# Kernel optimization log

Measured on AMD Instinct MI355X. Metric: run time of the kernel, lower is better.

The kernel has to match this reference:

```python
import jax, jax.numpy as jnp
import numpy as np

EPS = 1e-8  # torch F.cosine_similarity eps


def setup_inputs() -> dict:
    key = jax.random.key(0)
    k1, k2, k3 = jax.random.split(key, 3)
    bn, cn, dim = 4096, 8192, 1024
    x = jax.random.normal(k1, (bn, dim), dtype=jnp.float32)
    positive = jax.random.normal(k2, (bn, dim), dtype=jnp.float32)
    negative = jax.random.normal(k3, (cn, dim), dtype=jnp.float32)
    return {"x": x, "positive": positive, "negative": negative}


def reference(x, positive, negative):
    bn = x.shape[0]
    nx = jnp.linalg.norm(x, axis=1)          # (bn,)
    npos = jnp.linalg.norm(positive, axis=1)  # (bn,)
    nneg = jnp.linalg.norm(negative, axis=1)  # (cn,)
    # positive cosine similarity, torch-style eps clamp on norm product
    sim = jnp.sum(x * positive, axis=1) / jnp.maximum(nx * npos, EPS)  # (bn,)
    # negative cosine similarities via one matmul instead of (bn,cn,dim) repeats
    neg_sim = (x @ negative.T) / jnp.maximum(nx[:, None] * nneg[None, :], EPS)  # (bn,cn)
    p = jnp.exp(sim) / jnp.sum(jnp.exp(neg_sim), axis=1)  # (bn,)
    loss = -jnp.sum(jnp.log(p)) / bn
    return loss
```

## Files before the change

kernel.cpp:

```cpp
#include <hip/hip_runtime.h>
#include <stdint.h>
#include <stddef.h>

#define DIM 1024
#define EPS 1e-8f

typedef __attribute__((ext_vector_type(4))) float f32x4;
typedef __attribute__((ext_vector_type(2))) long longx2;

__device__ __forceinline__ void async_copy16(const void* g, void* l) {
    __builtin_amdgcn_global_load_lds(
        (__attribute__((address_space(1))) void*)const_cast<void*>(g),
        (__attribute__((address_space(3))) void*)(l), 16, 0, 0);
}

#define PIPE_SYNC(N) asm volatile("s_waitcnt vmcnt(" #N ")\n\ts_barrier" ::: "memory")

__global__ __launch_bounds__(256)
void prep_all(const float* __restrict__ x, const float* __restrict__ pos,
              const float* __restrict__ neg,
              unsigned char* __restrict__ Xn, unsigned char* __restrict__ Nn,
              float* __restrict__ simOut, float* __restrict__ rowsum, int bn) {
    const int lane = threadIdx.x & 63;
    const int wave = threadIdx.x >> 6;
    const int grow = blockIdx.x * 4 + wave;
    const bool isX = grow < bn;
    const int row  = isX ? grow : grow - bn;
    const float* src = isX ? x : neg;
    unsigned char* dst = isX ? Xn : Nn;

    const float4* s = (const float4*)(src + (size_t)row * DIM);
    float4 xv[4], pv[4];
    float sxx = 0.f, spp = 0.f, sxp = 0.f;
#pragma unroll
    for (int i = 0; i < 4; i++) {
        xv[i] = s[lane + 64 * i];
        sxx += xv[i].x * xv[i].x + xv[i].y * xv[i].y + xv[i].z * xv[i].z + xv[i].w * xv[i].w;
    }
    if (isX) {
        const float4* p = (const float4*)(pos + (size_t)row * DIM);
#pragma unroll
        for (int i = 0; i < 4; i++) {
            pv[i] = p[lane + 64 * i];
            spp += pv[i].x * pv[i].x + pv[i].y * pv[i].y + pv[i].z * pv[i].z + pv[i].w * pv[i].w;
            sxp += xv[i].x * pv[i].x + xv[i].y * pv[i].y + xv[i].z * pv[i].z + xv[i].w * pv[i].w;
        }
#pragma unroll
        for (int off = 1; off < 64; off <<= 1) {
            sxx += __shfl_xor(sxx, off);
            spp += __shfl_xor(spp, off);
            sxp += __shfl_xor(sxp, off);
        }
    } else {
#pragma unroll
        for (int off = 1; off < 64; off <<= 1) sxx += __shfl_xor(sxx, off);
    }
    const float nx  = sqrtf(sxx);
    const float inv = (nx > 0.f) ? (16.f / nx) : 0.f;
    if (isX && lane == 0) {
        const float np = sqrtf(spp);
        simOut[row] = sxp / fmaxf(nx * np, EPS);
        rowsum[row] = 0.f;
    }
    unsigned int t;
    t = __builtin_amdgcn_cvt_pk_fp8_f32(xv[0].x * inv, xv[0].y * inv, 0, false);
    unsigned int q0 = __builtin_amdgcn_cvt_pk_fp8_f32(xv[0].z * inv, xv[0].w * inv, t, true);
    t = __builtin_amdgcn_cvt_pk_fp8_f32(xv[1].x * inv, xv[1].y * inv, 0, false);
    unsigned int q1 = __builtin_amdgcn_cvt_pk_fp8_f32(xv[1].z * inv, xv[1].w * inv, t, true);
    t = __builtin_amdgcn_cvt_pk_fp8_f32(xv[2].x * inv, xv[2].y * inv, 0, false);
    unsigned int q2 = __builtin_amdgcn_cvt_pk_fp8_f32(xv[2].z * inv, xv[2].w * inv, t, true);
    t = __builtin_amdgcn_cvt_pk_fp8_f32(xv[3].x * inv, xv[3].y * inv, 0, false);
    unsigned int q3 = __builtin_amdgcn_cvt_pk_fp8_f32(xv[3].z * inv, xv[3].w * inv, t, true);

    const int m  = lane & 3;
    const int d0 = (m & 1) * 32 + (m >> 1) * 8;
    unsigned char* wbase = dst + (size_t)row * DIM + (lane >> 2) * 64;
    *(unsigned long long*)(wbase + d0)      = ((unsigned long long)q1 << 32) | q0;
    *(unsigned long long*)(wbase + d0 + 16) = ((unsigned long long)q3 << 32) | q2;
}

__global__ __launch_bounds__(256)
void gemm_exp_rowsum(const unsigned char* __restrict__ Xn,
                     const unsigned char* __restrict__ Nn,
                     float* __restrict__ rowsum) {
    constexpr int KB   = DIM;
    constexpr int BK   = 64;
    constexpr int BUFB = 128 * BK;
    __shared__ __align__(16) unsigned char Ash[3][BUFB];
    __shared__ __align__(16) unsigned char Bsh[3][BUFB];

    const int tid  = threadIdx.x;
    const int lane = tid & 63;
    const int wave = tid >> 6;
    const int rowBase = blockIdx.y * 128;
    const int colBase = blockIdx.x * 128;

    const int srow   = lane >> 2;
    const int schunk = (lane & 3) ^ ((srow >> 1) & 3);
    const unsigned char* gA = Xn + (size_t)(rowBase + wave * 16 + srow) * KB + schunk * 16;
    const unsigned char* gB = Nn + (size_t)(colBase + wave * 16 + srow) * KB + schunk * 16;
    const int lgrp0 = (wave * 16) * BK;
    const int lgrp1 = (wave * 16 + 64) * BK;

    const f32x4 fz = {0.f, 0.f, 0.f, 0.f};
    f32x4 acc[4][4];
#pragma unroll
    for (int mi = 0; mi < 4; mi++)
#pragma unroll
        for (int ni = 0; ni < 4; ni++) acc[mi][ni] = fz;

    const int m0   = (wave >> 1) * 64;
    const int n0   = (wave & 1) * 64;
    const int quad = lane >> 4;
    const int mrow = lane & 15;
    const int kx   = (mrow >> 1) & 3;

    int aoff[4], boff[4];
#pragma unroll
    for (int i = 0; i < 4; i++) {
        aoff[i] = (m0 + i * 16 + mrow) * BK + ((quad ^ kx) << 4);
        boff[i] = (n0 + i * 16 + mrow) * BK + ((quad ^ kx) << 4);
    }

#define STAGE(buf, stg)                                                  \
    do {                                                                 \
        const int kq = (stg) * BK;                                       \
        async_copy16(gA + kq,            &Ash[buf][lgrp0]);              \
        async_copy16(gA + 64 * KB + kq,  &Ash[buf][lgrp1]);              \
        async_copy16(gB + kq,            &Bsh[buf][lgrp0]);              \
        async_copy16(gB + 64 * KB + kq,  &Bsh[buf][lgrp1]);              \
    } while (0)

#define COMPUTE(buf)                                                     \
    do {                                                                 \
        longx2 a2[4], b2[4];                                             \
        _Pragma("unroll")                                                \
        for (int i = 0; i < 4; i++) {                                    \
            a2[i] = *(const longx2*)&Ash[buf][aoff[i]];                  \
            b2[i] = *(const longx2*)&Bsh[buf][boff[i]];                  \
        }                                                                \
        _Pragma("unroll")                                                \
        for (int mi = 0; mi < 4; mi++)                                   \
            _Pragma("unroll")                                            \
            for (int ni = 0; ni < 4; ni++) {                             \
                acc[mi][ni] = __builtin_amdgcn_mfma_f32_16x16x32_fp8_fp8( \
                    a2[mi].x, b2[ni].x, acc[mi][ni], 0, 0, 0);           \
                acc[mi][ni] = __builtin_amdgcn_mfma_f32_16x16x32_fp8_fp8( \
                    a2[mi].y, b2[ni].y, acc[mi][ni], 0, 0, 0);           \
            }                                                            \
    } while (0)

    STAGE(0, 0);
    STAGE(1, 1);
    for (int it = 0; it < 4; it++) {
        const int s = 3 * it + 2;
        PIPE_SYNC(4); STAGE(2, s);     COMPUTE(0);
        PIPE_SYNC(4); STAGE(0, s + 1); COMPUTE(1);
        PIPE_SYNC(4); STAGE(1, s + 2); COMPUTE(2);
    }
    PIPE_SYNC(4); STAGE(2, 14); COMPUTE(0);
    PIPE_SYNC(4); STAGE(0, 15); COMPUTE(1);
    PIPE_SYNC(4);               COMPUTE(2);
    PIPE_SYNC(0);               COMPUTE(0);
#undef STAGE
#undef COMPUTE

#pragma unroll
    for (int mi = 0; mi < 4; mi++) {
        float rs0 = 0.f, rs1 = 0.f, rs2 = 0.f, rs3 = 0.f;
#pragma unroll
        for (int ni = 0; ni < 4; ni++) {
            rs0 += __expf(acc[mi][ni].x * 0.00390625f);
            rs1 += __expf(acc[mi][ni].y * 0.00390625f);
            rs2 += __expf(acc[mi][ni].z * 0.00390625f);
            rs3 += __expf(acc[mi][ni].w * 0.00390625f);
        }
#pragma unroll
        for (int off = 1; off < 16; off <<= 1) {
            rs0 += __shfl_xor(rs0, off);
            rs1 += __shfl_xor(rs1, off);
            rs2 += __shfl_xor(rs2, off);
            rs3 += __shfl_xor(rs3, off);
        }
        if ((lane & 15) == 0) {
            const int r = rowBase + m0 + mi * 16 + quad * 4;
            atomicAdd(&rowsum[r + 0], rs0);
            atomicAdd(&rowsum[r + 1], rs1);
            atomicAdd(&rowsum[r + 2], rs2);
            atomicAdd(&rowsum[r + 3], rs3);
        }
    }
}

__global__ __launch_bounds__(1024)
void loss_kernel(const float* __restrict__ rowsum, const float* __restrict__ sim,
                 float* __restrict__ out, int bn) {
    const int tid  = threadIdx.x;
    const int lane = tid & 63;
    const int wave = tid >> 6;
    float acc = 0.f;
    for (int i = tid; i < bn; i += 1024) acc += logf(rowsum[i]) - sim[i];
#pragma unroll
    for (int off = 1; off < 64; off <<= 1) acc += __shfl_xor(acc, off);
    __shared__ float red[16];
    if (lane == 0) red[wave] = acc;
    __syncthreads();
    if (tid == 0) {
        float t = 0.f;
#pragma unroll
        for (int i = 0; i < 16; i++) t += red[i];
        out[0] = t / (float)bn;
    }
}

extern "C" void kernel_launch(void* const* d_in, const int* in_sizes, int n_in,
                              void* d_out, int out_size, void* d_ws, size_t ws_size,
                              hipStream_t stream) {
    const float* x   = (const float*)d_in[0];
    const float* pos = (const float*)d_in[1];
    const float* neg = (const float*)d_in[2];
    const int bn = in_sizes[0] / DIM;
    const int cn = in_sizes[2] / DIM;

    unsigned char* Xn = (unsigned char*)d_ws;
    unsigned char* Nn = Xn + (size_t)bn * DIM;
    float* sim    = (float*)(Nn + (size_t)cn * DIM);
    float* rowsum = sim + bn;

    prep_all<<<dim3((bn + cn) / 4), dim3(256), 0, stream>>>(x, pos, neg, Xn, Nn, sim, rowsum, bn);
    gemm_exp_rowsum<<<dim3(cn / 128, bn / 128), dim3(256), 0, stream>>>(Xn, Nn, rowsum);
    loss_kernel<<<dim3(1), dim3(1024), 0, stream>>>(rowsum, sim, (float*)d_out, bn);
}
```

Before: 166.8 us.

## Double-buffer GEMM pipeline and fuse final loss reduction into last block

The GEMM main loop goes from three LDS buffers to two. It waits on lgkmcnt after the fragment reads so the next async stage can be issued into the just-read buffer before the MFMAs. The separate single-block loss kernel is removed: a global done counter (reset in prep) elects the last finishing GEMM block to do the log-sum reduction. This saves a kernel launch and halves LDS use per block, which may raise occupancy, but it shortens prefetch distance and adds a serial tail reduction on one 256-thread block.

```diff
diff --git a/kernel.cpp b/kernel.cpp
--- a/kernel.cpp
+++ b/kernel.cpp
@@ -15,12 +15,14 @@
 }
 
 #define PIPE_SYNC(N) asm volatile("s_waitcnt vmcnt(" #N ")\n\ts_barrier" ::: "memory")
+#define LGK0() asm volatile("s_waitcnt lgkmcnt(0)" ::: "memory")
 
 __global__ __launch_bounds__(256)
 void prep_all(const float* __restrict__ x, const float* __restrict__ pos,
               const float* __restrict__ neg,
               unsigned char* __restrict__ Xn, unsigned char* __restrict__ Nn,
-              float* __restrict__ simOut, float* __restrict__ rowsum, int bn) {
+              float* __restrict__ simOut, float* __restrict__ rowsum,
+              int* __restrict__ done, int bn) {
     const int lane = threadIdx.x & 63;
     const int wave = threadIdx.x >> 6;
     const int grow = blockIdx.x * 4 + wave;
@@ -61,6 +63,7 @@
         const float np = sqrtf(spp);
         simOut[row] = sxp / fmaxf(nx * np, EPS);
         rowsum[row] = 0.f;
+        if (row == 0) *done = 0;
     }
     unsigned int t;
     t = __builtin_amdgcn_cvt_pk_fp8_f32(xv[0].x * inv, xv[0].y * inv, 0, false);
@@ -82,12 +85,14 @@
 __global__ __launch_bounds__(256)
 void gemm_exp_rowsum(const unsigned char* __restrict__ Xn,
                      const unsigned char* __restrict__ Nn,
-                     float* __restrict__ rowsum) {
+                     float* __restrict__ rowsum,
+                     const float* __restrict__ sim, float* __restrict__ out,
+                     int* __restrict__ done, int bn) {
     constexpr int KB   = DIM;
     constexpr int BK   = 64;
     constexpr int BUFB = 128 * BK;
-    __shared__ __align__(16) unsigned char Ash[3][BUFB];
-    __shared__ __align__(16) unsigned char Bsh[3][BUFB];
+    __shared__ __align__(16) unsigned char Ash[2][BUFB];
+    __shared__ __align__(16) unsigned char Bsh[2][BUFB];
 
     const int tid  = threadIdx.x;
     const int lane = tid & 63;
@@ -131,7 +136,7 @@
         async_copy16(gB + 64 * KB + kq,  &Bsh[buf][lgrp1]);              \
     } while (0)
 
-#define COMPUTE(buf)                                                     \
+#define PHASE(buf, STMT)                                                 \
     do {                                                                 \
         longx2 a2[4], b2[4];                                             \
         _Pragma("unroll")                                                \
@@ -139,6 +144,8 @@
             a2[i] = *(const longx2*)&Ash[buf][aoff[i]];                  \
             b2[i] = *(const longx2*)&Bsh[buf][boff[i]];                  \
         }                                                                \
+        LGK0();                                                          \
+        STMT;                                                            \
         _Pragma("unroll")                                                \
         for (int mi = 0; mi < 4; mi++)                                   \
             _Pragma("unroll")                                            \
@@ -152,18 +159,15 @@
 
     STAGE(0, 0);
     STAGE(1, 1);
-    for (int it = 0; it < 4; it++) {
-        const int s = 3 * it + 2;
-        PIPE_SYNC(4); STAGE(2, s);     COMPUTE(0);
-        PIPE_SYNC(4); STAGE(0, s + 1); COMPUTE(1);
-        PIPE_SYNC(4); STAGE(1, s + 2); COMPUTE(2);
-    }
-    PIPE_SYNC(4); STAGE(2, 14); COMPUTE(0);
-    PIPE_SYNC(4); STAGE(0, 15); COMPUTE(1);
-    PIPE_SYNC(4);               COMPUTE(2);
-    PIPE_SYNC(0);               COMPUTE(0);
+    for (int it = 0; it < 7; it++) {
+        const int s = 2 * it;
+        PIPE_SYNC(4); PHASE(0, STAGE(0, s + 2));
+        PIPE_SYNC(4); PHASE(1, STAGE(1, s + 3));
+    }
+    PIPE_SYNC(4); PHASE(0, (void)0);
+    PIPE_SYNC(0); PHASE(1, (void)0);
 #undef STAGE
-#undef COMPUTE
+#undef PHASE
 
 #pragma unroll
     for (int mi = 0; mi < 4; mi++) {
@@ -190,26 +194,23 @@
             atomicAdd(&rowsum[r + 3], rs3);
         }
     }
-}
-
-__global__ __launch_bounds__(1024)
-void loss_kernel(const float* __restrict__ rowsum, const float* __restrict__ sim,
-                 float* __restrict__ out, int bn) {
-    const int tid  = threadIdx.x;
-    const int lane = tid & 63;
-    const int wave = tid >> 6;
-    float acc = 0.f;
-    for (int i = tid; i < bn; i += 1024) acc += logf(rowsum[i]) - sim[i];
-#pragma unroll
-    for (int off = 1; off < 64; off <<= 1) acc += __shfl_xor(acc, off);
-    __shared__ float red[16];
-    if (lane == 0) red[wave] = acc;
+
+    int*   sflag = (int*)&Ash[0][0];
+    float* sred  = (float*)&Ash[0][64];
     __syncthreads();
-    if (tid == 0) {
-        float t = 0.f;
-#pragma unroll
-        for (int i = 0; i < 16; i++) t += red[i];
-        out[0] = t / (float)bn;
+    __threadfence();
+    if (tid == 0) *sflag = atomicAdd(done, 1);
+    __syncthreads();
+    if (*sflag == (int)(gridDim.x * gridDim.y) - 1) {
+        float acc2 = 0.f;
+        for (int i = tid; i < bn; i += 256)
+            acc2 += __logf(atomicAdd(&rowsum[i], 0.f)) - sim[i];
+#pragma unroll
+        for (int off = 1; off < 64; off <<= 1) acc2 += __shfl_xor(acc2, off);
+        if (lane == 0) sred[wave] = acc2;
+        __syncthreads();
+        if (tid == 0)
+            out[0] = (sred[0] + sred[1] + sred[2] + sred[3]) / (float)bn;
     }
 }
 
@@ -226,8 +227,10 @@
     unsigned char* Nn = Xn + (size_t)bn * DIM;
     float* sim    = (float*)(Nn + (size_t)cn * DIM);
     float* rowsum = sim + bn;
-
-    prep_all<<<dim3((bn + cn) / 4), dim3(256), 0, stream>>>(x, pos, neg, Xn, Nn, sim, rowsum, bn);
-    gemm_exp_rowsum<<<dim3(cn / 128, bn / 128), dim3(256), 0, stream>>>(Xn, Nn, rowsum);
-    loss_kernel<<<dim3(1), dim3(1024), 0, stream>>>(rowsum, sim, (float*)d_out, bn);
-}
+    int*   done   = (int*)(rowsum + bn);
+
+    prep_all<<<dim3((bn + cn) / 4), dim3(256), 0, stream>>>(
+        x, pos, neg, Xn, Nn, sim, rowsum, done, bn);
+    gemm_exp_rowsum<<<dim3(cn / 128, bn / 128), dim3(256), 0, stream>>>(
+        Xn, Nn, rowsum, sim, (float*)d_out, done, bn);
+}
```

Result: slower. 310.9 us (+86.4%).

## Enlarge GEMM block tile to 256x128 with 8 waves and double buffering

Applied to the files above, without the earlier changes.

The fp8 GEMM block now covers 256 rows of X by 128 negatives using 512 threads (8 waves), so each B tile loaded into LDS is reused by twice as many rows. This is meant to cut global and LDS load traffic per MFMA. The triple-buffered pipeline, which used explicit vmcnt waits, is replaced by a simpler double-buffered loop synchronised with __syncthreads. That gives less load-latency hiding, and the larger block may lower occupancy.

```diff
diff --git a/kernel.cpp b/kernel.cpp
--- a/kernel.cpp
+++ b/kernel.cpp
@@ -13,8 +13,6 @@
         (__attribute__((address_space(1))) void*)const_cast<void*>(g),
         (__attribute__((address_space(3))) void*)(l), 16, 0, 0);
 }
-
-#define PIPE_SYNC(N) asm volatile("s_waitcnt vmcnt(" #N ")\n\ts_barrier" ::: "memory")
 
 __global__ __launch_bounds__(256)
 void prep_all(const float* __restrict__ x, const float* __restrict__ pos,
@@ -79,28 +77,29 @@
     *(unsigned long long*)(wbase + d0 + 16) = ((unsigned long long)q3 << 32) | q2;
 }
 
-__global__ __launch_bounds__(256)
+__global__ __launch_bounds__(512, 4)
 void gemm_exp_rowsum(const unsigned char* __restrict__ Xn,
                      const unsigned char* __restrict__ Nn,
                      float* __restrict__ rowsum) {
-    constexpr int KB   = DIM;
-    constexpr int BK   = 64;
-    constexpr int BUFB = 128 * BK;
-    __shared__ __align__(16) unsigned char Ash[3][BUFB];
-    __shared__ __align__(16) unsigned char Bsh[3][BUFB];
+    constexpr int KB = DIM;
+    constexpr int BK = 64;
+    __shared__ __align__(16) unsigned char Ash[2][256 * BK];
+    __shared__ __align__(16) unsigned char Bsh[2][128 * BK];
 
     const int tid  = threadIdx.x;
     const int lane = tid & 63;
     const int wave = tid >> 6;
-    const int rowBase = blockIdx.y * 128;
+    const int rowBase = blockIdx.y * 256;
     const int colBase = blockIdx.x * 128;
 
     const int srow   = lane >> 2;
     const int schunk = (lane & 3) ^ ((srow >> 1) & 3);
-    const unsigned char* gA = Xn + (size_t)(rowBase + wave * 16 + srow) * KB + schunk * 16;
-    const unsigned char* gB = Nn + (size_t)(colBase + wave * 16 + srow) * KB + schunk * 16;
-    const int lgrp0 = (wave * 16) * BK;
-    const int lgrp1 = (wave * 16 + 64) * BK;
+    const unsigned char* gA0 = Xn + (size_t)(rowBase +       wave * 16 + srow) * KB + schunk * 16;
+    const unsigned char* gA1 = Xn + (size_t)(rowBase + 128 + wave * 16 + srow) * KB + schunk * 16;
+    const unsigned char* gB  = Nn + (size_t)(colBase +       wave * 16 + srow) * KB + schunk * 16;
+    const int lgA0 = (wave * 16) * BK;
+    const int lgA1 = (wave * 16 + 128) * BK;
+    const int lgB  = (wave * 16) * BK;
 
     const f32x4 fz = {0.f, 0.f, 0.f, 0.f};
     f32x4 acc[4][4];
@@ -125,10 +124,9 @@
 #define STAGE(buf, stg)                                                  \
     do {                                                                 \
         const int kq = (stg) * BK;                                       \
-        async_copy16(gA + kq,            &Ash[buf][lgrp0]);              \
-        async_copy16(gA + 64 * KB + kq,  &Ash[buf][lgrp1]);              \
-        async_copy16(gB + kq,            &Bsh[buf][lgrp0]);              \
-        async_copy16(gB + 64 * KB + kq,  &Bsh[buf][lgrp1]);              \
+        async_copy16(gA0 + kq, &Ash[buf][lgA0]);                         \
+        async_copy16(gA1 + kq, &Ash[buf][lgA1]);                         \
+        async_copy16(gB  + kq, &Bsh[buf][lgB]);                          \
     } while (0)
 
 #define COMPUTE(buf)                                                     \
@@ -151,17 +149,15 @@
     } while (0)
 
     STAGE(0, 0);
-    STAGE(1, 1);
-    for (int it = 0; it < 4; it++) {
-        const int s = 3 * it + 2;
-        PIPE_SYNC(4); STAGE(2, s);     COMPUTE(0);
-        PIPE_SYNC(4); STAGE(0, s + 1); COMPUTE(1);
-        PIPE_SYNC(4); STAGE(1, s + 2); COMPUTE(2);
-    }
-    PIPE_SYNC(4); STAGE(2, 14); COMPUTE(0);
-    PIPE_SYNC(4); STAGE(0, 15); COMPUTE(1);
-    PIPE_SYNC(4);               COMPUTE(2);
-    PIPE_SYNC(0);               COMPUTE(0);
+#pragma unroll 1
+    for (int it = 0; it < 8; it++) {
+        __syncthreads();
+        STAGE(1, 2 * it + 1);
+        COMPUTE(0);
+        __syncthreads();
+        if (it < 7) STAGE(0, 2 * it + 2);
+        COMPUTE(1);
+    }
 #undef STAGE
 #undef COMPUTE
 
@@ -227,7 +223,8 @@
     float* sim    = (float*)(Nn + (size_t)cn * DIM);
     float* rowsum = sim + bn;
 
-    prep_all<<<dim3((bn + cn) / 4), dim3(256), 0, stream>>>(x, pos, neg, Xn, Nn, sim, rowsum, bn);
-    gemm_exp_rowsum<<<dim3(cn / 128, bn / 128), dim3(256), 0, stream>>>(Xn, Nn, rowsum);
+    prep_all<<<dim3((bn + cn) / 4), dim3(256), 0, stream>>>(
+        x, pos, neg, Xn, Nn, sim, rowsum, bn);
+    gemm_exp_rowsum<<<dim3(cn / 128, bn / 256), dim3(512), 0, stream>>>(Xn, Nn, rowsum);
     loss_kernel<<<dim3(1), dim3(1024), 0, stream>>>(rowsum, sim, (float*)d_out, bn);
 }
```

After: 176.8 us. 1.06x slower.
